# Performance work log

Hardware: AMD Instinct MI355X
Metric: run time of the kernel (lower is better)

## Reference

```python
import jax, jax.numpy as jnp
import numpy as np

B = 65536

def setup_inputs() -> dict:
    key = jax.random.key(0)
    ks = jax.random.split(key, 6)
    x = jax.random.normal(ks[0], (B, 784), dtype=jnp.float32)
    w_conv = jnp.ones((3, 3), dtype=jnp.float32)  # Parameter(ones((3,3)))
    w1 = jax.random.normal(ks[1], (676, 256), dtype=jnp.float32) * 0.04
    b1 = jax.random.normal(ks[2], (256,), dtype=jnp.float32) * 0.01
    w2 = jax.random.normal(ks[3], (256, 10), dtype=jnp.float32) * 0.06
    b2 = jax.random.normal(ks[4], (10,), dtype=jnp.float32) * 0.01
    return {"x": x, "w_conv": w_conv, "w1": w1, "b1": b1, "w2": w2, "b2": b2}

def reference(x, w_conv, w1, b1, w2, b2):
    b = x.shape[0]
    img = x.reshape(b, 1, 28, 28)
    # Convolve() is cross-correlation (no kernel flip), 'VALID': 28->26
    kern = w_conv.reshape(1, 1, 3, 3)
    conv = jax.lax.conv_general_dilated(
        img, kern, window_strides=(1, 1), padding='VALID',
        dimension_numbers=('NCHW', 'OIHW', 'NCHW'))  # (B,1,26,26)
    feat = conv.reshape(b, 676)
    h = jax.nn.relu(feat @ w1 + b1)  # (B,256)
    return h @ w2 + b2               # (B,10)
```

## Files before the change

kernel.cpp:

```cpp
#include <hip/hip_runtime.h>
#include <hip/hip_bf16.h>
#include <stdint.h>

typedef __bf16 bf16;
typedef __attribute__((ext_vector_type(8))) __bf16 bf16x8;
typedef __attribute__((ext_vector_type(4))) float f32x4;

#define KREAL 784
#define NTILES 25
#define TROW   40
#define TILE_ELEMS (256 * TROW)

#define GLOBAL_AS __attribute__((address_space(1)))
#define LDS_AS    __attribute__((address_space(3)))

__global__ __launch_bounds__(256) void prep_w1tt(const float* __restrict__ w_conv,
                                                 const float* __restrict__ w1,
                                                 bf16* __restrict__ W) {
    const int tile = blockIdx.x / TROW;
    const int kk   = blockIdx.x % TROW;
    const int n    = threadIdx.x;
    const int k    = tile * 32 + kk;
    float s = 0.0f;
    if (kk < 32 && k < KREAL) {
        const int r = k / 28, c = k % 28;
        #pragma unroll
        for (int di = 0; di < 3; ++di) {
            const int i = r - di;
            if (i < 0 || i >= 26) continue;
            #pragma unroll
            for (int dj = 0; dj < 3; ++dj) {
                const int j = c - dj;
                if (j < 0 || j >= 26) continue;
                s += w_conv[di * 3 + dj] * w1[(i * 26 + j) * 256 + n];
            }
        }
    }
    W[(size_t)tile * TILE_ELEMS + n * TROW + kk] = (bf16)s;
}

__global__ __launch_bounds__(256, 2) void fused_mlp(
    const float* __restrict__ x,
    const bf16*  __restrict__ W,
    const float* __restrict__ b1,
    const float* __restrict__ w2,
    const float* __restrict__ b2,
    float* __restrict__ out)
{
    __shared__ bf16  Bs[2][TILE_ELEMS];
    __shared__ float w2s[256][10];
    __shared__ float b1s[256];
    __shared__ float b2s[10];

    const int t    = threadIdx.x;
    const int wave = t >> 6;
    const int lane = t & 63;
    const int c    = lane & 15;
    const int q    = lane >> 4;

    const int row0 = blockIdx.x * 128;

    for (int i = t; i < 2560; i += 256) ((float*)w2s)[i] = w2[i];
    b1s[t] = b1[t];
    if (t < 10) b2s[t] = b2[t];

    const float* arow0 = x + (size_t)(row0 + wave * 32 + c) * KREAL + q * 8;
    const float* arow1 = arow0 + (size_t)16 * KREAL;
    const bf16* bsrc = W + (size_t)(wave * 5) * 512 + lane * 8;

    f32x4 acc[2][16];
    #pragma unroll
    for (int mt = 0; mt < 2; ++mt)
        #pragma unroll
        for (int nt = 0; nt < 16; ++nt)
            acc[mt][nt] = (f32x4){0.f, 0.f, 0.f, 0.f};

    #pragma unroll
    for (int j = 0; j < 5; ++j) {
        __builtin_amdgcn_global_load_lds(
            (const GLOBAL_AS void*)(bsrc + j * 512),
            (LDS_AS void*)((char*)&Bs[0][0] + (wave * 5 + j) * 1024), 16, 0, 0);
    }
    float4 f0a = *(const float4*)arow0, f0b = *(const float4*)(arow0 + 4);
    float4 f1a = *(const float4*)arow1, f1b = *(const float4*)(arow1 + 4);
    bf16x8 a0, a1;
    a0[0] = (bf16)f0a.x; a0[1] = (bf16)f0a.y; a0[2] = (bf16)f0a.z; a0[3] = (bf16)f0a.w;
    a0[4] = (bf16)f0b.x; a0[5] = (bf16)f0b.y; a0[6] = (bf16)f0b.z; a0[7] = (bf16)f0b.w;
    a1[0] = (bf16)f1a.x; a1[1] = (bf16)f1a.y; a1[2] = (bf16)f1a.z; a1[3] = (bf16)f1a.w;
    a1[4] = (bf16)f1b.x; a1[5] = (bf16)f1b.y; a1[6] = (bf16)f1b.z; a1[7] = (bf16)f1b.w;
    __syncthreads();

    #pragma unroll 1
    for (int it = 0; it < NTILES; ++it) {
        const int cur = it & 1;
        const bool more = (it + 1) < NTILES;

        if (more) {
            const bf16* bs = bsrc + (size_t)(it + 1) * TILE_ELEMS;
            char* bd = (char*)&Bs[cur ^ 1][0] + wave * 5 * 1024;
            #pragma unroll
            for (int j = 0; j < 5; ++j) {
                __builtin_amdgcn_global_load_lds(
                    (const GLOBAL_AS void*)(bs + j * 512),
                    (LDS_AS void*)(bd + j * 1024), 16, 0, 0);
            }
            const int kn = (it + 1) * 32;
            if (kn + q * 8 < KREAL) {
                const float* p0 = arow0 + kn;
                const float* p1 = arow1 + kn;
                f0a = *(const float4*)p0; f0b = *(const float4*)(p0 + 4);
                f1a = *(const float4*)p1; f1b = *(const float4*)(p1 + 4);
            } else {
                f0a = f0b = f1a = f1b = (float4){0.f, 0.f, 0.f, 0.f};
            }
        }

        #pragma unroll
        for (int nt = 0; nt < 16; ++nt) {
            bf16x8 b = *(const bf16x8*)&Bs[cur][(nt * 16 + c) * TROW + q * 8];
            acc[0][nt] = __builtin_amdgcn_mfma_f32_16x16x32_bf16(a0, b, acc[0][nt], 0, 0, 0);
            acc[1][nt] = __builtin_amdgcn_mfma_f32_16x16x32_bf16(a1, b, acc[1][nt], 0, 0, 0);
        }

        if (more) {
            a0[0] = (bf16)f0a.x; a0[1] = (bf16)f0a.y; a0[2] = (bf16)f0a.z; a0[3] = (bf16)f0a.w;
            a0[4] = (bf16)f0b.x; a0[5] = (bf16)f0b.y; a0[6] = (bf16)f0b.z; a0[7] = (bf16)f0b.w;
            a1[0] = (bf16)f1a.x; a1[1] = (bf16)f1a.y; a1[2] = (bf16)f1a.z; a1[3] = (bf16)f1a.w;
            a1[4] = (bf16)f1b.x; a1[5] = (bf16)f1b.y; a1[6] = (bf16)f1b.z; a1[7] = (bf16)f1b.w;
        }

        __syncthreads();
    }

    float bl[16];
    #pragma unroll
    for (int nt = 0; nt < 16; ++nt) bl[nt] = b1s[nt * 16 + c];

    #pragma unroll
    for (int mt = 0; mt < 2; ++mt)
        #pragma unroll
        for (int nt = 0; nt < 16; ++nt)
            #pragma unroll
            for (int r = 0; r < 4; ++r) {
                float v = acc[mt][nt][r] + bl[nt];
                acc[mt][nt][r] = v > 0.f ? v : 0.f;
            }

    #pragma unroll 1
    for (int j = 0; j < 10; ++j) {
        float wj[16];
        #pragma unroll
        for (int nt = 0; nt < 16; ++nt) wj[nt] = w2s[nt * 16 + c][j];
        const float b2j = b2s[j];
        #pragma unroll
        for (int mt = 0; mt < 2; ++mt)
            #pragma unroll
            for (int r = 0; r < 4; ++r) {
                float s = 0.f;
                #pragma unroll
                for (int nt = 0; nt < 16; ++nt) s += acc[mt][nt][r] * wj[nt];
                s += __shfl_xor(s, 1, 64);
                s += __shfl_xor(s, 2, 64);
                s += __shfl_xor(s, 4, 64);
                s += __shfl_xor(s, 8, 64);
                if (c == j) {
                    const int row = row0 + wave * 32 + mt * 16 + q * 4 + r;
                    out[(size_t)row * 10 + j] = s + b2j;
                }
            }
    }
}

extern "C" void kernel_launch(void* const* d_in, const int* in_sizes, int n_in,
                              void* d_out, int out_size, void* d_ws, size_t ws_size,
                              hipStream_t stream) {
    const float* x  = (const float*)d_in[0];
    const float* wc = (const float*)d_in[1];
    const float* w1 = (const float*)d_in[2];
    const float* b1 = (const float*)d_in[3];
    const float* w2 = (const float*)d_in[4];
    const float* b2 = (const float*)d_in[5];
    float* out = (float*)d_out;
    bf16* W = (bf16*)d_ws;

    prep_w1tt<<<dim3(NTILES * TROW), dim3(256), 0, stream>>>(wc, w1, W);
    fused_mlp<<<dim3(65536 / 128), dim3(256), 0, stream>>>(x, W, b1, w2, b2, out);
}
```

Baseline: 317.0 us.

## Replace double-buffered K loop with single-buffered 64-wide K steps

```diff
diff --git a/kernel.cpp b/kernel.cpp
--- a/kernel.cpp
+++ b/kernel.cpp
@@ -7,9 +7,10 @@
 typedef __attribute__((ext_vector_type(4))) float f32x4;
 
 #define KREAL 784
-#define NTILES 25
+#define NTILES 26
 #define TROW   40
 #define TILE_ELEMS (256 * TROW)
+#define NPER   13
 
 #define GLOBAL_AS __attribute__((address_space(1)))
 #define LDS_AS    __attribute__((address_space(3)))
@@ -47,7 +48,7 @@
     const float* __restrict__ b2,
     float* __restrict__ out)
 {
-    __shared__ bf16  Bs[2][TILE_ELEMS];
+    __shared__ bf16  Ws[2 * TILE_ELEMS];
     __shared__ float w2s[256][10];
     __shared__ float b1s[256];
     __shared__ float b2s[10];
@@ -66,7 +67,8 @@
 
     const float* arow0 = x + (size_t)(row0 + wave * 32 + c) * KREAL + q * 8;
     const float* arow1 = arow0 + (size_t)16 * KREAL;
-    const bf16* bsrc = W + (size_t)(wave * 5) * 512 + lane * 8;
+    const bf16* bsrc = W + (size_t)wave * 10 * 512 + lane * 8;
+    char* bdst = (char*)&Ws[0] + wave * 10 * 1024;
 
     f32x4 acc[2][16];
     #pragma unroll
@@ -75,61 +77,64 @@
         for (int nt = 0; nt < 16; ++nt)
             acc[mt][nt] = (f32x4){0.f, 0.f, 0.f, 0.f};
 
-    #pragma unroll
-    for (int j = 0; j < 5; ++j) {
-        __builtin_amdgcn_global_load_lds(
-            (const GLOBAL_AS void*)(bsrc + j * 512),
-            (LDS_AS void*)((char*)&Bs[0][0] + (wave * 5 + j) * 1024), 16, 0, 0);
-    }
-    float4 f0a = *(const float4*)arow0, f0b = *(const float4*)(arow0 + 4);
-    float4 f1a = *(const float4*)arow1, f1b = *(const float4*)(arow1 + 4);
-    bf16x8 a0, a1;
-    a0[0] = (bf16)f0a.x; a0[1] = (bf16)f0a.y; a0[2] = (bf16)f0a.z; a0[3] = (bf16)f0a.w;
-    a0[4] = (bf16)f0b.x; a0[5] = (bf16)f0b.y; a0[6] = (bf16)f0b.z; a0[7] = (bf16)f0b.w;
-    a1[0] = (bf16)f1a.x; a1[1] = (bf16)f1a.y; a1[2] = (bf16)f1a.z; a1[3] = (bf16)f1a.w;
-    a1[4] = (bf16)f1b.x; a1[5] = (bf16)f1b.y; a1[6] = (bf16)f1b.z; a1[7] = (bf16)f1b.w;
-    __syncthreads();
+    #pragma unroll 1
+    for (int p = 0; p < NPER; ++p) {
+        const int k0 = p * 64;
 
-    #pragma unroll 1
-    for (int it = 0; it < NTILES; ++it) {
-        const int cur = it & 1;
-        const bool more = (it + 1) < NTILES;
+        __syncthreads();
 
-        if (more) {
-            const bf16* bs = bsrc + (size_t)(it + 1) * TILE_ELEMS;
-            char* bd = (char*)&Bs[cur ^ 1][0] + wave * 5 * 1024;
+        float4 s0r0a, s0r0b, s0r1a, s0r1b, s1r0a, s1r0b, s1r1a, s1r1b;
+        if (k0 + q * 8 < KREAL) {
+            const float* p0 = arow0 + k0;
+            const float* p1 = arow1 + k0;
+            s0r0a = *(const float4*)p0; s0r0b = *(const float4*)(p0 + 4);
+            s0r1a = *(const float4*)p1; s0r1b = *(const float4*)(p1 + 4);
+        } else {
+            s0r0a = s0r0b = s0r1a = s0r1b = (float4){0.f, 0.f, 0.f, 0.f};
+        }
+        if (k0 + 32 + q * 8 < KREAL) {
+            const float* p0 = arow0 + k0 + 32;
+            const float* p1 = arow1 + k0 + 32;
+            s1r0a = *(const float4*)p0; s1r0b = *(const float4*)(p0 + 4);
+            s1r1a = *(const float4*)p1; s1r1b = *(const float4*)(p1 + 4);
+        } else {
+            s1r0a = s1r0b = s1r1a = s1r1b = (float4){0.f, 0.f, 0.f, 0.f};
+        }
+
+        {
+            const bf16* bs = bsrc + (size_t)p * 2 * TILE_ELEMS;
             #pragma unroll
-            for (int j = 0; j < 5; ++j) {
+            for (int j = 0; j < 10; ++j) {
                 __builtin_amdgcn_global_load_lds(
                     (const GLOBAL_AS void*)(bs + j * 512),
-                    (LDS_AS void*)(bd + j * 1024), 16, 0, 0);
-            }
-            const int kn = (it + 1) * 32;
-            if (kn + q * 8 < KREAL) {
-                const float* p0 = arow0 + kn;
-                const float* p1 = arow1 + kn;
-                f0a = *(const float4*)p0; f0b = *(const float4*)(p0 + 4);
-                f1a = *(const float4*)p1; f1b = *(const float4*)(p1 + 4);
-            } else {
-                f0a = f0b = f1a = f1b = (float4){0.f, 0.f, 0.f, 0.f};
+                    (LDS_AS void*)(bdst + j * 1024), 16, 0, 0);
             }
         }
 
+        __syncthreads();
+
+        bf16x8 a00, a01, a10, a11;
+        a00[0] = (bf16)s0r0a.x; a00[1] = (bf16)s0r0a.y; a00[2] = (bf16)s0r0a.z; a00[3] = (bf16)s0r0a.w;
+        a00[4] = (bf16)s0r0b.x; a00[5] = (bf16)s0r0b.y; a00[6] = (bf16)s0r0b.z; a00[7] = (bf16)s0r0b.w;
+        a01[0] = (bf16)s0r1a.x; a01[1] = (bf16)s0r1a.y; a01[2] = (bf16)s0r1a.z; a01[3] = (bf16)s0r1a.w;
+        a01[4] = (bf16)s0r1b.x; a01[5] = (bf16)s0r1b.y; a01[6] = (bf16)s0r1b.z; a01[7] = (bf16)s0r1b.w;
+        a10[0] = (bf16)s1r0a.x; a10[1] = (bf16)s1r0a.y; a10[2] = (bf16)s1r0a.z; a10[3] = (bf16)s1r0a.w;
+        a10[4] = (bf16)s1r0b.x; a10[5] = (bf16)s1r0b.y; a10[6] = (bf16)s1r0b.z; a10[7] = (bf16)s1r0b.w;
+        a11[0] = (bf16)s1r1a.x; a11[1] = (bf16)s1r1a.y; a11[2] = (bf16)s1r1a.z; a11[3] = (bf16)s1r1a.w;
+        a11[4] = (bf16)s1r1b.x; a11[5] = (bf16)s1r1b.y; a11[6] = (bf16)s1r1b.z; a11[7] = (bf16)s1r1b.w;
+
         #pragma unroll
         for (int nt = 0; nt < 16; ++nt) {
-            bf16x8 b = *(const bf16x8*)&Bs[cur][(nt * 16 + c) * TROW + q * 8];
-            acc[0][nt] = __builtin_amdgcn_mfma_f32_16x16x32_bf16(a0, b, acc[0][nt], 0, 0, 0);
-            acc[1][nt] = __builtin_amdgcn_mfma_f32_16x16x32_bf16(a1, b, acc[1][nt], 0, 0, 0);
+            bf16x8 b0 = *(const bf16x8*)&Ws[(nt * 16 + c) * TROW + q * 8];
+            acc[0][nt] = __builtin_amdgcn_mfma_f32_16x16x32_bf16(a00, b0, acc[0][nt], 0, 0, 0);
+            acc[1][nt] = __builtin_amdgcn_mfma_f32_16x16x32_bf16(a01, b0, acc[1][nt], 0, 0, 0);
         }
-
-        if (more) {
-            a0[0] = (bf16)f0a.x; a0[1] = (bf16)f0a.y; a0[2] = (bf16)f0a.z; a0[3] = (bf16)f0a.w;
-            a0[4] = (bf16)f0b.x; a0[5] = (bf16)f0b.y; a0[6] = (bf16)f0b.z; a0[7] = (bf16)f0b.w;
-            a1[0] = (bf16)f1a.x; a1[1] = (bf16)f1a.y; a1[2] = (bf16)f1a.z; a1[3] = (bf16)f1a.w;
-            a1[4] = (bf16)f1b.x; a1[5] = (bf16)f1b.y; a1[6] = (bf16)f1b.z; a1[7] = (bf16)f1b.w;
+        #pragma unroll
+        for (int nt = 0; nt < 16; ++nt) {
+            bf16x8 b1f = *(const bf16x8*)&Ws[TILE_ELEMS + (nt * 16 + c) * TROW + q * 8];
+            acc[0][nt] = __builtin_amdgcn_mfma_f32_16x16x32_bf16(a10, b1f, acc[0][nt], 0, 0, 0);
+            acc[1][nt] = __builtin_amdgcn_mfma_f32_16x16x32_bf16(a11, b1f, acc[1][nt], 0, 0, 0);
         }
-
-        __syncthreads();
     }
 
     float bl[16];
```

After: 328.7 us. 3.7% more time.
